# Optimization experiments

Measured on AMD Instinct MI355X. Metric: run time of the kernel, lower is better.

The kernel has to match this reference:

```python
import jax, jax.numpy as jnp
import numpy as np

S, B, H, Dh = 3072, 1, 16, 64

def setup_inputs() -> dict:
    key = jax.random.key(0)
    kq, kk, kv, km = jax.random.split(key, 4)
    query = jax.random.normal(kq, (S, B, H, Dh), dtype=jnp.float32)
    key_t = jax.random.normal(kk, (S, B, H, Dh), dtype=jnp.float32)
    value = jax.random.normal(kv, (S, B, H, Dh), dtype=jnp.float32)
    attention_mask = jax.random.randint(km, (1, 1, S, S), 0, 2).astype(bool)  # True = keep
    return {"query": query, "key": key_t, "value": value,
            "attention_mask": attention_mask, "attn_mask_type": 0}

def reference(query, key, value, attention_mask, attn_mask_type):
    # sbhd -> bshd
    q = jnp.transpose(query, (1, 0, 2, 3))   # (B,Sq,H,D)
    k = jnp.transpose(key,   (1, 0, 2, 3))   # (B,Sk,H,D)
    v = jnp.transpose(value, (1, 0, 2, 3))   # (B,Sk,H,D)
    scale = 1.0 / jnp.sqrt(jnp.asarray(q.shape[-1], q.dtype))
    scores = jnp.einsum('bqhd,bkhd->bhqk', q, k) * scale  # (B,H,Sq,Sk)
    scores = jnp.where(attention_mask, scores, -jnp.inf)  # bool mask, True=keep
    attn = jax.nn.softmax(scores, axis=-1)
    out = jnp.einsum('bhqk,bkhd->bqhd', attn, v)           # (B,Sq,H,D)
    return out
```

## Files before the change

kernel.cpp:

```cpp
#include <hip/hip_runtime.h>
#include <stdint.h>

#define SEQ 3072
#define NH  16
#define DH  64
#define WQ  32
#define KVBLK 64
#define NKT (SEQ / KVBLK)
#define HALF_T (NKT / 2)
#define NQT (SEQ / WQ)
#define NWORDS (SEQ * SEQ / 64)

typedef __attribute__((ext_vector_type(8))) __bf16 bf16x8;
typedef __attribute__((ext_vector_type(16))) float f32x16;

union BF8 { ushort us[8]; uint u[4]; uint4 u4; bf16x8 v; };

__device__ __forceinline__ ushort f2bf(float f) {
    uint u = __builtin_bit_cast(uint, f);
    return (ushort)((u + 0x7FFFu + ((u >> 16) & 1u)) >> 16);
}

__global__ void detect_kernel(const uint32_t* __restrict__ m, int* __restrict__ flag) {
    __shared__ int cntA, cntB;
    if (threadIdx.x == 0) { cntA = 0; cntB = 0; }
    __syncthreads();
    int a = 0, b = 0;
    for (int i = 0; i < 16; ++i) {
        uint32_t w = m[threadIdx.x + i * 256];
        if (w & 0xFFFFFF00u) a = 1;
        if (w & 0x0000FFFFu) b = 1;
    }
    if (a) atomicOr(&cntA, 1);
    if (b) atomicOr(&cntB, 1);
    __syncthreads();
    if (threadIdx.x == 0) *flag = (cntA == 0) ? 1 : ((cntB == 0) ? 2 : 0);
}

#define SCALE_Q (0.125f * 1.44269504f)

__global__ __launch_bounds__(256)
void fused_prep(const float* __restrict__ K, const float* __restrict__ V,
                const float* __restrict__ Q, const void* __restrict__ mask,
                const int* __restrict__ flag,
                ushort* __restrict__ Kbz, ushort* __restrict__ Vtz,
                ushort* __restrict__ Qb, uint64_t* __restrict__ bits)
{
    const int b = blockIdx.x;
    const int tid = threadIdx.x;

    if (b < 768) {
        const int kt = b % NKT, h = b / NKT;
        __shared__ float Vf[64][68];
        {
            const int kr = tid >> 2, dc = (tid & 3) * 16;
            const float* vsrc = V + (((size_t)(kt * KVBLK + kr) * NH + h) * DH + dc);
            #pragma unroll
            for (int j = 0; j < 4; ++j) {
                float4 t = *(const float4*)(vsrc + 4 * j);
                Vf[kr][dc + 4 * j + 0] = t.x; Vf[kr][dc + 4 * j + 1] = t.y;
                Vf[kr][dc + 4 * j + 2] = t.z; Vf[kr][dc + 4 * j + 3] = t.w;
            }
        }

        ushort* kout = Kbz + ((size_t)(h * NKT + kt)) * 4096;
        #pragma unroll
        for (int i = 0; i < 2; ++i) {
            const int idx = tid + 256 * i;
            const int f = idx >> 6, l = idx & 63;
            const int kc = f >> 1, kh = f & 1;
            const int row = kh * 32 + (l & 31);
            const int kcol = kc * 16 + (l >> 5) * 8;
            const float* ks = K + (((size_t)(kt * KVBLK + row) * NH + h) * DH + kcol);
            float4 a = *(const float4*)(ks);
            float4 c = *(const float4*)(ks + 4);
            BF8 t;
            t.us[0] = f2bf(a.x); t.us[1] = f2bf(a.y); t.us[2] = f2bf(a.z); t.us[3] = f2bf(a.w);
            t.us[4] = f2bf(c.x); t.us[5] = f2bf(c.y); t.us[6] = f2bf(c.z); t.us[7] = f2bf(c.w);
            *(uint4*)(kout + idx * 8) = t.u4;
        }

        __syncthreads();

        ushort* vout = Vtz + ((size_t)(h * NKT + kt)) * 4096;
        #pragma unroll
        for (int i = 0; i < 2; ++i) {
            const int idx = tid + 256 * i;
            const int f = idx >> 6, l = idx & 63;
            const int kc = f >> 1, dh = f & 1;
            const int d = dh * 32 + (l & 31);
            const int kr0 = kc * 16 + (l >> 5) * 8;
            BF8 t;
            #pragma unroll
            for (int j = 0; j < 8; ++j)
                t.us[j] = f2bf(Vf[kr0 + j][d]);
            *(uint4*)(vout + idx * 8) = t.u4;
        }
    } else if (b < 1024) {
        for (int vb = b - 768; vb < SEQ * NH * DH / (256 * 8); vb += 256) {
            int i = (vb * 256 + tid) * 8;
            float4 a = *(const float4*)(Q + i);
            float4 c = *(const float4*)(Q + i + 4);
            BF8 t;
            t.us[0] = f2bf(a.x * SCALE_Q); t.us[1] = f2bf(a.y * SCALE_Q);
            t.us[2] = f2bf(a.z * SCALE_Q); t.us[3] = f2bf(a.w * SCALE_Q);
            t.us[4] = f2bf(c.x * SCALE_Q); t.us[5] = f2bf(c.y * SCALE_Q);
            t.us[6] = f2bf(c.z * SCALE_Q); t.us[7] = f2bf(c.w * SCALE_Q);
            *(uint4*)(Qb + i) = t.u4;
        }
    } else {
        const int f = *flag;
        for (int vb = b - 1024; vb < SEQ * SEQ / 256; vb += 1024) {
            const int g = vb * 256 + tid;
            bool v;
            if (f == 1)      v = ((const int*)mask)[g] != 0;
            else if (f == 2) v = ((const float*)mask)[g] != 0.0f;
            else             v = ((const unsigned char*)mask)[g] != 0;
            uint64_t bl = __ballot(v);
            if ((tid & 63) == 0) {
                int w = g >> 6;
                int qrow = w / NKT, cw = w % NKT;
                bits[(size_t)cw * SEQ + qrow] = bl;
            }
        }
    }
}

__device__ __forceinline__ bf16x8 ldfrag(const ushort* tile, int f, int lane) {
    return *(const bf16x8*)(tile + f * 512 + lane * 8);
}

__device__ __forceinline__ void process_tile(
    const bf16x8 kf[8], const bf16x8 vf[8], const bf16x8 qf[4],
    uint64_t mw, int hh, f32x16& o0, f32x16& o1, float& l_)
{
    const uint64_t mu = mw >> (4 * hh);
    const uint mlo = (uint)mu, mhi = (uint)(mu >> 32);
    f32x16 s0, s1;
    #pragma unroll
    for (int r = 0; r < 16; ++r) {
        const int sh = (r & 3) + 8 * (r >> 2);
        const uint b0 = (mlo >> sh) & 1u;
        const uint b1 = (mhi >> sh) & 1u;
        s0[r] = __builtin_bit_cast(float, (b0 - 1u) & 0xFF800000u);
        s1[r] = __builtin_bit_cast(float, (b1 - 1u) & 0xFF800000u);
    }

    __builtin_amdgcn_s_setprio(1);
    #pragma unroll
    for (int kc = 0; kc < 4; ++kc) {
        s0 = __builtin_amdgcn_mfma_f32_32x32x16_bf16(kf[kc * 2 + 0], qf[kc], s0, 0, 0, 0);
        s1 = __builtin_amdgcn_mfma_f32_32x32x16_bf16(kf[kc * 2 + 1], qf[kc], s1, 0, 0, 0);
    }
    __builtin_amdgcn_s_setprio(0);

    float la0 = 0.f, la1 = 0.f;
    #pragma unroll
    for (int r = 0; r < 16; ++r) {
        float p0 = __builtin_amdgcn_exp2f(s0[r]);
        float p1 = __builtin_amdgcn_exp2f(s1[r]);
        s0[r] = p0; s1[r] = p1;
        la0 += p0; la1 += p1;
    }
    l_ += la0 + la1;

    bf16x8 pa[4];
    {
        #define PKSWAP(dlo, dhi, a0, a1, b0, b1)                                   \
            {   uint wl, wh;                                                       \
                asm("v_cvt_pk_bf16_f32 %0, %1, %2" : "=v"(wl) : "v"(a0), "v"(a1)); \
                asm("v_cvt_pk_bf16_f32 %0, %1, %2" : "=v"(wh) : "v"(b0), "v"(b1)); \
                asm("v_permlane32_swap_b32 %0, %1" : "+v"(wl), "+v"(wh));          \
                dlo = wl; dhi = wh; }
        BF8 t0, t1, t2, t3;
        PKSWAP(t0.u[0], t0.u[2], s0[0],  s0[1],  s0[4],  s0[5]);
        PKSWAP(t0.u[1], t0.u[3], s0[2],  s0[3],  s0[6],  s0[7]);
        PKSWAP(t1.u[0], t1.u[2], s0[8],  s0[9],  s0[12], s0[13]);
        PKSWAP(t1.u[1], t1.u[3], s0[10], s0[11], s0[14], s0[15]);
        PKSWAP(t2.u[0], t2.u[2], s1[0],  s1[1],  s1[4],  s1[5]);
        PKSWAP(t2.u[1], t2.u[3], s1[2],  s1[3],  s1[6],  s1[7]);
        PKSWAP(t3.u[0], t3.u[2], s1[8],  s1[9],  s1[12], s1[13]);
        PKSWAP(t3.u[1], t3.u[3], s1[10], s1[11], s1[14], s1[15]);
        pa[0] = t0.v; pa[1] = t1.v; pa[2] = t2.v; pa[3] = t3.v;
        #undef PKSWAP
    }

    __builtin_amdgcn_s_setprio(1);
    #pragma unroll
    for (int kc = 0; kc < 4; ++kc) {
        o0 = __builtin_amdgcn_mfma_f32_32x32x16_bf16(pa[kc], vf[kc * 2 + 0], o0, 0, 0, 0);
        o1 = __builtin_amdgcn_mfma_f32_32x32x16_bf16(pa[kc], vf[kc * 2 + 1], o1, 0, 0, 0);
    }
    __builtin_amdgcn_s_setprio(0);
}

__global__ __launch_bounds__(256, 2)
void attn16(const ushort* __restrict__ Qb, const ushort* __restrict__ Kbz,
            const ushort* __restrict__ Vtz, const uint64_t* __restrict__ bits2,
            float* __restrict__ out)
{
    const int bid = blockIdx.x;
    const int swz = (bid & 7) * 96 + (bid >> 3);
    const int h = swz / 48, qg = swz % 48;
    const int tid = threadIdx.x;
    const int wv = tid >> 6, lane = tid & 63;
    const int qsub = wv & 1, kvh = wv >> 1;
    const int lq = lane & 31, hh = lane >> 5;
    const int qrow0 = (qg * 2 + qsub) * WQ;

    __shared__ __align__(16) float MergeF[2][2368];

    bf16x8 qf[4];
    {
        const ushort* qp = Qb + ((size_t)(qrow0 + lq) * NH + h) * DH;
        #pragma unroll
        for (int kc = 0; kc < 4; ++kc)
            qf[kc] = *(const bf16x8*)(qp + kc * 16 + hh * 8);
    }

    f32x16 o0, o1;
    #pragma unroll
    for (int i = 0; i < 16; ++i) { o0[i] = 0.f; o1[i] = 0.f; }
    float l_ = 0.f;

    const int kt0 = kvh * HALF_T;
    const ushort* kbase = Kbz + ((size_t)(h * NKT + kt0)) * 4096;
    const ushort* vbase = Vtz + ((size_t)(h * NKT + kt0)) * 4096;
    const uint64_t* bb = bits2 + (size_t)kt0 * SEQ + qrow0 + lq;

    bf16x8 kA[8], kB[8], vC[8];

    #pragma unroll
    for (int f = 0; f < 8; ++f) kA[f] = ldfrag(kbase, f, lane);
    uint64_t mwA = bb[0];

    for (int it = 0; it < HALF_T; it += 2) {
        {
            const ushort* vt = vbase + (size_t)it * 4096;
            #pragma unroll
            for (int f = 0; f < 8; ++f) vC[f] = ldfrag(vt, f, lane);
            const ushort* kn = kbase + (size_t)(it + 1) * 4096;
            #pragma unroll
            for (int f = 0; f < 8; ++f) kB[f] = ldfrag(kn, f, lane);
            const uint64_t mwB = bb[(size_t)(it + 1) * SEQ];
            process_tile(kA, vC, qf, mwA, hh, o0, o1, l_);
            mwA = mwB;
        }
        {
            const int t2 = (it + 2 < HALF_T) ? it + 2 : HALF_T - 1;
            const ushort* vt = vbase + (size_t)(it + 1) * 4096;
            #pragma unroll
            for (int f = 0; f < 8; ++f) vC[f] = ldfrag(vt, f, lane);
            const ushort* kn = kbase + (size_t)t2 * 4096;
            #pragma unroll
            for (int f = 0; f < 8; ++f) kA[f] = ldfrag(kn, f, lane);
            const uint64_t mwN = bb[(size_t)t2 * SEQ];
            process_tile(kB, vC, qf, mwA, hh, o0, o1, l_);
            mwA = mwN;
        }
    }

    {
        float a = l_, b = l_;
        asm("v_permlane32_swap_b32 %0, %1" : "+v"(a), "+v"(b));
        l_ = a + b;
    }

    float* LMq = &MergeF[qsub][0];
    if (kvh == 1) {
        if (hh == 0) LMq[64 * 36 + lq] = l_;
        #pragma unroll
        for (int j = 0; j < 4; ++j) {
            float4 t0, t1;
            t0.x = o0[4 * j]; t0.y = o0[4 * j + 1]; t0.z = o0[4 * j + 2]; t0.w = o0[4 * j + 3];
            t1.x = o1[4 * j]; t1.y = o1[4 * j + 1]; t1.z = o1[4 * j + 2]; t1.w = o1[4 * j + 3];
            *(float4*)&LMq[lq * 36 + 4 * hh + 8 * j]        = t0;
            *(float4*)&LMq[(lq + 32) * 36 + 4 * hh + 8 * j] = t1;
        }
    }
    __syncthreads();
    if (kvh == 0) {
        const float lB = LMq[64 * 36 + lq];
        const float l = l_ + lB;
        const float inv = (l > 0.f) ? 1.0f / l : 0.f;
        #pragma unroll
        for (int r = 0; r < 16; ++r) {
            const int q_r = (r & 3) + 8 * (r >> 2) + 4 * hh;
            const float ir = __shfl(inv, q_r);
            float* op = out + ((size_t)(qrow0 + q_r) * NH + h) * DH;
            op[lq]      = (o0[r] + LMq[lq * 36 + q_r]) * ir;
            op[lq + 32] = (o1[r] + LMq[(lq + 32) * 36 + q_r]) * ir;
        }
    }
}

__global__ __launch_bounds__(256, 2)
void attn_fb(const float* __restrict__ Q, const float* __restrict__ K,
             const float* __restrict__ V, const int* __restrict__ mask_i32,
             float* __restrict__ out)
{
    const int qtile = blockIdx.x, h = blockIdx.y;
    const int tid  = threadIdx.x;
    const int wv   = tid >> 6, lane = tid & 63;
    const int g    = lane >> 4, c = lane & 15;
    const int qb   = qtile * 64 + wv * 16;

    typedef __attribute__((ext_vector_type(4))) float f32x4;
    __shared__ __align__(16) ushort KbS[KVBLK * 72];
    __shared__ __align__(16) ushort VtS[DH * 72];
    __shared__ __align__(16) ushort PbS[4 * 16 * 72];
    ushort* Pw = &PbS[wv * 16 * 72];

    bf16x8 qa[2];
    {
        const float* qp = Q + ((qb + c) * NH + h) * DH;
        #pragma unroll
        for (int kk = 0; kk < 2; ++kk) {
            BF8 t;
            const float4* pp = (const float4*)(qp + kk * 32 + g * 8);
            float4 f0 = pp[0], f1 = pp[1];
            t.us[0] = f2bf(f0.x * 0.125f); t.us[1] = f2bf(f0.y * 0.125f);
            t.us[2] = f2bf(f0.z * 0.125f); t.us[3] = f2bf(f0.w * 0.125f);
            t.us[4] = f2bf(f1.x * 0.125f); t.us[5] = f2bf(f1.y * 0.125f);
            t.us[6] = f2bf(f1.z * 0.125f); t.us[7] = f2bf(f1.w * 0.125f);
            qa[kk] = t.v;
        }
    }

    f32x4 oacc[4];
    float m_[4], lsum[4];
    #pragma unroll
    for (int nt = 0; nt < 4; ++nt) oacc[nt] = (f32x4){0.f, 0.f, 0.f, 0.f};
    #pragma unroll
    for (int r = 0; r < 4; ++r) { m_[r] = -1e30f; lsum[r] = 0.f; }

    const int srow0 = tid >> 3;
    const int fch   = tid & 7;

    for (int kt = 0; kt < NKT; ++kt) {
        __syncthreads();
        #pragma unroll
        for (int i = 0; i < 2; ++i) {
            const int krow = srow0 + 32 * i;
            const int gofs = ((kt * KVBLK + krow) * NH + h) * DH + fch * 8;
            const float4* kp = (const float4*)(K + gofs);
            const float4* vp = (const float4*)(V + gofs);
            float4 k0 = kp[0], k1 = kp[1];
            float4 v0 = vp[0], v1 = vp[1];
            BF8 kb;
            kb.us[0] = f2bf(k0.x); kb.us[1] = f2bf(k0.y);
            kb.us[2] = f2bf(k0.z); kb.us[3] = f2bf(k0.w);
            kb.us[4] = f2bf(k1.x); kb.us[5] = f2bf(k1.y);
            kb.us[6] = f2bf(k1.z); kb.us[7] = f2bf(k1.w);
            *(uint4*)&KbS[krow * 72 + (fch ^ (krow & 7)) * 8] = kb.u4;
            float vf[8] = {v0.x, v0.y, v0.z, v0.w, v1.x, v1.y, v1.z, v1.w};
            #pragma unroll
            for (int j = 0; j < 8; ++j) {
                const int d = fch * 8 + j;
                VtS[d * 72 + ((krow >> 3) ^ ((d >> 3) & 7)) * 8 + (krow & 7)] = f2bf(vf[j]);
            }
        }
        __syncthreads();

        f32x4 sacc[4];
        #pragma unroll
        for (int nt = 0; nt < 4; ++nt) sacc[nt] = (f32x4){0.f, 0.f, 0.f, 0.f};
        #pragma unroll
        for (int kk = 0; kk < 2; ++kk) {
            #pragma unroll
            for (int nt = 0; nt < 4; ++nt) {
                const int krow = nt * 16 + c;
                bf16x8 kf = *(const bf16x8*)&KbS[krow * 72 + (((g + 4 * kk) ^ (krow & 7))) * 8];
                sacc[nt] = __builtin_amdgcn_mfma_f32_16x16x32_bf16(qa[kk], kf, sacc[nt], 0, 0, 0);
            }
        }

        float pmax[4];
        #pragma unroll
        for (int r = 0; r < 4; ++r) pmax[r] = -1e30f;
        #pragma unroll
        for (int nt = 0; nt < 4; ++nt) {
            #pragma unroll
            for (int r = 0; r < 4; ++r) {
                bool keep = mask_i32[(size_t)(qb + 4 * g + r) * SEQ + kt * KVBLK + nt * 16 + c] != 0;
                float s = keep ? sacc[nt][r] : -1e30f;
                sacc[nt][r] = s;
                pmax[r] = fmaxf(pmax[r], s);
            }
        }
        #pragma unroll
        for (int r = 0; r < 4; ++r) {
            float v = pmax[r];
            v = fmaxf(v, __shfl_xor(v, 1));
            v = fmaxf(v, __shfl_xor(v, 2));
            v = fmaxf(v, __shfl_xor(v, 4));
            v = fmaxf(v, __shfl_xor(v, 8));
            float nm = fmaxf(m_[r], v);
            float alpha = __expf(m_[r] - nm);
            m_[r] = nm;
            lsum[r] *= alpha;
            #pragma unroll
            for (int nt = 0; nt < 4; ++nt) oacc[nt][r] *= alpha;
        }
        #pragma unroll
        for (int nt = 0; nt < 4; ++nt) {
            #pragma unroll
            for (int r = 0; r < 4; ++r) {
                float pv = __expf(sacc[nt][r] - m_[r]);
                lsum[r] += pv;
                const int row = 4 * g + r, col = nt * 16 + c;
                Pw[row * 72 + (((col >> 3) ^ (row & 7))) * 8 + (col & 7)] = f2bf(pv);
            }
        }
        #pragma unroll
        for (int kk = 0; kk < 2; ++kk) {
            bf16x8 pa = *(const bf16x8*)&Pw[c * 72 + (((g + 4 * kk) ^ (c & 7))) * 8];
            #pragma unroll
            for (int nt = 0; nt < 4; ++nt) {
                const int d = nt * 16 + c;
                bf16x8 vb = *(const bf16x8*)&VtS[d * 72 + (((g + 4 * kk) ^ ((d >> 3) & 7))) * 8];
                oacc[nt] = __builtin_amdgcn_mfma_f32_16x16x32_bf16(pa, vb, oacc[nt], 0, 0, 0);
            }
        }
    }

    #pragma unroll
    for (int r = 0; r < 4; ++r) {
        float v = lsum[r];
        v += __shfl_xor(v, 1); v += __shfl_xor(v, 2);
        v += __shfl_xor(v, 4); v += __shfl_xor(v, 8);
        lsum[r] = (v > 0.f) ? 1.0f / v : 0.f;
    }
    #pragma unroll
    for (int nt = 0; nt < 4; ++nt) {
        #pragma unroll
        for (int r = 0; r < 4; ++r) {
            out[((qb + 4 * g + r) * NH + h) * DH + nt * 16 + c] = oacc[nt][r] * lsum[r];
        }
    }
}

extern "C" void kernel_launch(void* const* d_in, const int* in_sizes, int n_in,
                              void* d_out, int out_size, void* d_ws, size_t ws_size,
                              hipStream_t stream) {
    const float* Q    = (const float*)d_in[0];
    const float* K    = (const float*)d_in[1];
    const float* V    = (const float*)d_in[2];
    const void*  mask = d_in[3];
    float* out = (float*)d_out;

    const size_t off_bits = 64;
    const size_t off_qb   = off_bits + (size_t)NWORDS * 8;
    const size_t off_kbz  = off_qb  + (size_t)SEQ * NH * DH * 2;
    const size_t off_vtz  = off_kbz + (size_t)SEQ * NH * DH * 2;
    const size_t need     = off_vtz + (size_t)SEQ * NH * DH * 2;

    if (ws_size >= need) {
        int*      flag = (int*)d_ws;
        uint64_t* bits = (uint64_t*)((char*)d_ws + off_bits);
        ushort*   Qb   = (ushort*)((char*)d_ws + off_qb);
        ushort*   Kbz  = (ushort*)((char*)d_ws + off_kbz);
        ushort*   Vtz  = (ushort*)((char*)d_ws + off_vtz);
        detect_kernel<<<1, 256, 0, stream>>>((const uint32_t*)mask, flag);
        fused_prep<<<2048, 256, 0, stream>>>(K, V, Q, mask, flag, Kbz, Vtz, Qb, bits);
        attn16<<<NQT * NH / 2, 256, 0, stream>>>(Qb, Kbz, Vtz, bits, out);
    } else {
        attn_fb<<<dim3(NKT, NH), 256, 0, stream>>>(Q, K, V, (const int*)mask, out);
    }
}
```

Baseline: 92.88 us.

## Drop K double-buffering in attention loop to raise occupancy to three blocks

Replaces the software-pipelined loop, which prefetched the next K tile and mask word while processing the current one, with a simple per-tile load-then-compute loop. It also raises launch bounds from 2 to 3 blocks per CU. Freeing the kB register buffer lowers VGPR pressure so more waves can hide memory latency. The trade-off is losing explicit prefetch overlap inside each wave, so loads now sit directly in front of each tile's MFMAs. The grid of 768 blocks is unchanged.

```diff
diff --git a/kernel.cpp b/kernel.cpp
--- a/kernel.cpp
+++ b/kernel.cpp
@@ -194,8 +194,8 @@
     __builtin_amdgcn_s_setprio(0);
 }
 
-__global__ __launch_bounds__(256, 2)
-void attn16(const ushort* __restrict__ Qb, const ushort* __restrict__ Kbz,
+__global__ __launch_bounds__(256, 3)
+void attn17(const ushort* __restrict__ Qb, const ushort* __restrict__ Kbz,
             const ushort* __restrict__ Vtz, const uint64_t* __restrict__ bits2,
             float* __restrict__ out)
 {
@@ -228,36 +228,16 @@
     const ushort* vbase = Vtz + ((size_t)(h * NKT + kt0)) * 4096;
     const uint64_t* bb = bits2 + (size_t)kt0 * SEQ + qrow0 + lq;
 
-    bf16x8 kA[8], kB[8], vC[8];
-
-    #pragma unroll
-    for (int f = 0; f < 8; ++f) kA[f] = ldfrag(kbase, f, lane);
-    uint64_t mwA = bb[0];
-
-    for (int it = 0; it < HALF_T; it += 2) {
-        {
-            const ushort* vt = vbase + (size_t)it * 4096;
-            #pragma unroll
-            for (int f = 0; f < 8; ++f) vC[f] = ldfrag(vt, f, lane);
-            const ushort* kn = kbase + (size_t)(it + 1) * 4096;
-            #pragma unroll
-            for (int f = 0; f < 8; ++f) kB[f] = ldfrag(kn, f, lane);
-            const uint64_t mwB = bb[(size_t)(it + 1) * SEQ];
-            process_tile(kA, vC, qf, mwA, hh, o0, o1, l_);
-            mwA = mwB;
-        }
-        {
-            const int t2 = (it + 2 < HALF_T) ? it + 2 : HALF_T - 1;
-            const ushort* vt = vbase + (size_t)(it + 1) * 4096;
-            #pragma unroll
-            for (int f = 0; f < 8; ++f) vC[f] = ldfrag(vt, f, lane);
-            const ushort* kn = kbase + (size_t)t2 * 4096;
-            #pragma unroll
-            for (int f = 0; f < 8; ++f) kA[f] = ldfrag(kn, f, lane);
-            const uint64_t mwN = bb[(size_t)t2 * SEQ];
-            process_tile(kB, vC, qf, mwA, hh, o0, o1, l_);
-            mwA = mwN;
-        }
+    for (int it = 0; it < HALF_T; ++it) {
+        const ushort* kt_ = kbase + (size_t)it * 4096;
+        const ushort* vt_ = vbase + (size_t)it * 4096;
+        bf16x8 kA[8], vC[8];
+        #pragma unroll
+        for (int f = 0; f < 8; ++f) kA[f] = ldfrag(kt_, f, lane);
+        #pragma unroll
+        for (int f = 0; f < 8; ++f) vC[f] = ldfrag(vt_, f, lane);
+        const uint64_t mw = bb[(size_t)it * SEQ];
+        process_tile(kA, vC, qf, mw, hh, o0, o1, l_);
     }
 
     {
@@ -463,7 +443,7 @@
         ushort*   Vtz  = (ushort*)((char*)d_ws + off_vtz);
         detect_kernel<<<1, 256, 0, stream>>>((const uint32_t*)mask, flag);
         fused_prep<<<2048, 256, 0, stream>>>(K, V, Q, mask, flag, Kbz, Vtz, Qb, bits);
-        attn16<<<NQT * NH / 2, 256, 0, stream>>>(Qb, Kbz, Vtz, bits, out);
+        attn17<<<NQT * NH / 2, 256, 0, stream>>>(Qb, Kbz, Vtz, bits, out);
     } else {
         attn_fb<<<dim3(NKT, NH), 256, 0, stream>>>(Q, K, V, (const int*)mask, out);
     }
```

Result: no change. 94.40 us (+1.6%).

## Split KV range across four wave pairs per block instead of two

Applied to the files above, without the earlier changes.

Doubles the block to 512 threads so each query tile's KV sequence is split into four quarters processed by separate wave pairs, then merged through shared memory. This increases waves per CU and shortens each wave's serial KV loop, which should improve latency hiding. In exchange it adds a larger LDS merge buffer (about 57 KB), three-way partial accumulation in the final reduction, and possible register pressure under the 512-thread launch bound.

```diff
diff --git a/kernel.cpp b/kernel.cpp
--- a/kernel.cpp
+++ b/kernel.cpp
@@ -7,7 +7,7 @@
 #define WQ  32
 #define KVBLK 64
 #define NKT (SEQ / KVBLK)
-#define HALF_T (NKT / 2)
+#define QUART_T (NKT / 4)
 #define NQT (SEQ / WQ)
 #define NWORDS (SEQ * SEQ / 64)
 
@@ -194,8 +194,8 @@
     __builtin_amdgcn_s_setprio(0);
 }
 
-__global__ __launch_bounds__(256, 2)
-void attn16(const ushort* __restrict__ Qb, const ushort* __restrict__ Kbz,
+__global__ __launch_bounds__(512, 2)
+void attn19(const ushort* __restrict__ Qb, const ushort* __restrict__ Kbz,
             const ushort* __restrict__ Vtz, const uint64_t* __restrict__ bits2,
             float* __restrict__ out)
 {
@@ -204,11 +204,11 @@
     const int h = swz / 48, qg = swz % 48;
     const int tid = threadIdx.x;
     const int wv = tid >> 6, lane = tid & 63;
-    const int qsub = wv & 1, kvh = wv >> 1;
+    const int qsub = wv & 1, kvq = wv >> 1;
     const int lq = lane & 31, hh = lane >> 5;
     const int qrow0 = (qg * 2 + qsub) * WQ;
 
-    __shared__ __align__(16) float MergeF[2][2368];
+    __shared__ __align__(16) float MergeF[2][3][2368];
 
     bf16x8 qf[4];
     {
@@ -223,7 +223,7 @@
     for (int i = 0; i < 16; ++i) { o0[i] = 0.f; o1[i] = 0.f; }
     float l_ = 0.f;
 
-    const int kt0 = kvh * HALF_T;
+    const int kt0 = kvq * QUART_T;
     const ushort* kbase = Kbz + ((size_t)(h * NKT + kt0)) * 4096;
     const ushort* vbase = Vtz + ((size_t)(h * NKT + kt0)) * 4096;
     const uint64_t* bb = bits2 + (size_t)kt0 * SEQ + qrow0 + lq;
@@ -234,7 +234,7 @@
     for (int f = 0; f < 8; ++f) kA[f] = ldfrag(kbase, f, lane);
     uint64_t mwA = bb[0];
 
-    for (int it = 0; it < HALF_T; it += 2) {
+    for (int it = 0; it < QUART_T; it += 2) {
         {
             const ushort* vt = vbase + (size_t)it * 4096;
             #pragma unroll
@@ -247,7 +247,7 @@
             mwA = mwB;
         }
         {
-            const int t2 = (it + 2 < HALF_T) ? it + 2 : HALF_T - 1;
+            const int t2 = (it + 2 < QUART_T) ? it + 2 : QUART_T - 1;
             const ushort* vt = vbase + (size_t)(it + 1) * 4096;
             #pragma unroll
             for (int f = 0; f < 8; ++f) vC[f] = ldfrag(vt, f, lane);
@@ -266,30 +266,37 @@
         l_ = a + b;
     }
 
-    float* LMq = &MergeF[qsub][0];
-    if (kvh == 1) {
-        if (hh == 0) LMq[64 * 36 + lq] = l_;
+    if (kvq >= 1) {
+        float* dst = &MergeF[qsub][kvq - 1][0];
+        if (hh == 0) dst[64 * 36 + lq] = l_;
         #pragma unroll
         for (int j = 0; j < 4; ++j) {
             float4 t0, t1;
             t0.x = o0[4 * j]; t0.y = o0[4 * j + 1]; t0.z = o0[4 * j + 2]; t0.w = o0[4 * j + 3];
             t1.x = o1[4 * j]; t1.y = o1[4 * j + 1]; t1.z = o1[4 * j + 2]; t1.w = o1[4 * j + 3];
-            *(float4*)&LMq[lq * 36 + 4 * hh + 8 * j]        = t0;
-            *(float4*)&LMq[(lq + 32) * 36 + 4 * hh + 8 * j] = t1;
+            *(float4*)&dst[lq * 36 + 4 * hh + 8 * j]        = t0;
+            *(float4*)&dst[(lq + 32) * 36 + 4 * hh + 8 * j] = t1;
         }
     }
     __syncthreads();
-    if (kvh == 0) {
-        const float lB = LMq[64 * 36 + lq];
-        const float l = l_ + lB;
+    if (kvq == 0) {
+        float l = l_;
+        #pragma unroll
+        for (int p = 0; p < 3; ++p) l += MergeF[qsub][p][64 * 36 + lq];
         const float inv = (l > 0.f) ? 1.0f / l : 0.f;
         #pragma unroll
         for (int r = 0; r < 16; ++r) {
             const int q_r = (r & 3) + 8 * (r >> 2) + 4 * hh;
             const float ir = __shfl(inv, q_r);
+            float a0 = o0[r], a1 = o1[r];
+            #pragma unroll
+            for (int p = 0; p < 3; ++p) {
+                a0 += MergeF[qsub][p][lq * 36 + q_r];
+                a1 += MergeF[qsub][p][(lq + 32) * 36 + q_r];
+            }
             float* op = out + ((size_t)(qrow0 + q_r) * NH + h) * DH;
-            op[lq]      = (o0[r] + LMq[lq * 36 + q_r]) * ir;
-            op[lq + 32] = (o1[r] + LMq[(lq + 32) * 36 + q_r]) * ir;
+            op[lq]      = a0 * ir;
+            op[lq + 32] = a1 * ir;
         }
     }
 }
@@ -463,7 +470,7 @@
         ushort*   Vtz  = (ushort*)((char*)d_ws + off_vtz);
         detect_kernel<<<1, 256, 0, stream>>>((const uint32_t*)mask, flag);
         fused_prep<<<2048, 256, 0, stream>>>(K, V, Q, mask, flag, Kbz, Vtz, Qb, bits);
-        attn16<<<NQT * NH / 2, 256, 0, stream>>>(Qb, Kbz, Vtz, bits, out);
+        attn19<<<768, 512, 0, stream>>>(Qb, Kbz, Vtz, bits, out);
     } else {
         attn_fb<<<dim3(NKT, NH), 256, 0, stream>>>(Q, K, V, (const int*)mask, out);
     }
```

After: 97.90 us. 1.05x slower.
